# Kernel tuning notes

Measured on AMD Instinct MI355X. Metric: run time of the kernel, lower is better.

Reference implementation:

```python
import jax, jax.numpy as jnp
import numpy as np

R = 4  # num_relations


def rgcn_conv(x, src, dst, etype, W, root, bias):
    """PyG RGCNConv (aggr='mean', no self-loops):
    out_i = x_i @ root + bias + sum_r mean_{j in N_r(i)} (x_j @ W_r)
    x: [N,D], W: [R,D,H], root: [D,H], bias: [H]
    """
    N = x.shape[0]
    Rr, _, H = W.shape
    x_r = jnp.einsum('nd,rdh->rnh', x, W)          # [R,N,H] relation-transformed feats
    msg = x_r[etype, src]                          # [E,H] per-edge messages
    seg = etype * N + dst                          # combined (relation, dst) segment id
    sums = jax.ops.segment_sum(msg, seg, num_segments=Rr * N)            # [R*N,H]
    cnt = jax.ops.segment_sum(jnp.ones(msg.shape[0], msg.dtype), seg,
                              num_segments=Rr * N)                        # [R*N]
    mean = sums / jnp.maximum(cnt, 1.0)[:, None]
    agg = mean.reshape(Rr, N, H).sum(0)            # sum over relations
    return agg + x @ root + bias


def setup_inputs() -> dict:
    key = jax.random.key(0)
    ks = jax.random.split(key, 12)
    N, E, D, H, ED = 20000, 320000, 256, 256, 64
    s = lambda fan: 1.0 / np.sqrt(fan)
    return {
        'x': jax.random.normal(ks[0], (N, D), jnp.float32),
        'edge_index': jax.random.randint(ks[1], (2, E), 0, N),
        'edge_type': jax.random.randint(ks[2], (E,), 0, R),
        'edge_attr': jax.random.normal(ks[3], (E, ED), jnp.float32),
        'W0': jax.random.normal(ks[4], (R, D, H), jnp.float32) * s(D),
        'root0': jax.random.normal(ks[5], (D, H), jnp.float32) * s(D),
        'b0': jnp.zeros((H,), jnp.float32),
        'W1': jax.random.normal(ks[6], (R, H, H), jnp.float32) * s(H),
        'root1': jax.random.normal(ks[7], (H, H), jnp.float32) * s(H),
        'b1': jnp.zeros((H,), jnp.float32),
        'lin_w': jax.random.normal(ks[8], (H, 2), jnp.float32) * s(H),
        'lin_b': jnp.zeros((2,), jnp.float32),
    }


def reference(x, edge_index, edge_type, edge_attr, W0, root0, b0, W1, root1, b1, lin_w, lin_b):
    src, dst = edge_index[0], edge_index[1]
    h = jax.nn.relu(rgcn_conv(x, src, dst, edge_type, W0, root0, b0))
    h = rgcn_conv(h, src, dst, edge_type, W1, root1, b1)
    g = h.sum(axis=0, keepdims=True)   # global_add_pool, single graph -> [1,H]
    # dropout inactive in eval mode
    return g @ lin_w + lin_b           # [1,2]
```

## Files before the change

### kernel.cpp

```cpp
#include <hip/hip_runtime.h>
#include <hip/hip_bf16.h>

#define RREL 4
#define DIM 256
#define KDIM 1280
#define KMEAN 1024
#define BCAP 32

__device__ __forceinline__ float bf2f(unsigned short u) {
    union { unsigned int i; float f; } z; z.i = ((unsigned int)u) << 16; return z.f;
}
__device__ __forceinline__ unsigned short f2bf(float f) {
    __hip_bfloat16 h = __float2bfloat16(f);
    return *(unsigned short*)&h;
}

typedef __attribute__((ext_vector_type(8))) short bf16x8;
typedef __attribute__((ext_vector_type(8))) unsigned short u16x8;
typedef __attribute__((ext_vector_type(4))) float f32x4;
typedef __attribute__((ext_vector_type(4))) float fx4;


__global__ __launch_bounds__(256)
void prep(const int* __restrict__ etype, const int* __restrict__ src,
          const int* __restrict__ dst,
          int* __restrict__ counts, int* __restrict__ bucket, int N, int E,
          const float* __restrict__ x, __hip_bfloat16* __restrict__ xb, int n4,
          const float* __restrict__ W0, const float* __restrict__ root0,
          __hip_bfloat16* __restrict__ WT,
          int eb, int cb) {
    int b = blockIdx.x;
    if (b < eb) {
        int e = b * 256 + threadIdx.x;
        if (e < E) {
            int seg = etype[e] * N + dst[e];
            int p = atomicAdd(&counts[seg], 1);
            if (p < BCAP) bucket[(size_t)seg * BCAP + p] = src[e];
        }
    } else if (b < eb + cb) {
        int i = (b - eb) * 256 + threadIdx.x;
        if (i < n4) {
            fx4 v = *((const fx4*)x + i);
            ushort4 u = make_ushort4(f2bf(v.x), f2bf(v.y), f2bf(v.z), f2bf(v.w));
            ((ushort4*)xb)[i] = u;
        }
    } else {
        __shared__ float tile[32][33];
        int q = b - eb - cb;
        int nblk = q / 40;
        int kblk = q - nblk * 40;
        int k0 = kblk * 32, n0 = nblk * 32;
        int tx = threadIdx.x & 31, ty = threadIdx.x >> 5;
        const float* srcp;
        int kbase;
        if (k0 < RREL * DIM) { srcp = W0; kbase = k0; } else { srcp = root0; kbase = k0 - RREL * DIM; }
#pragma unroll
        for (int j = 0; j < 4; j++) {
            int k = kbase + ty + j * 8;
            tile[ty + j * 8][tx] = srcp[(size_t)k * DIM + n0 + tx];
        }
        __syncthreads();
#pragma unroll
        for (int j = 0; j < 4; j++) {
            int n = n0 + ty + j * 8;
            WT[(size_t)n * KDIM + k0 + tx] = __float2bfloat16(tile[tx][ty + j * 8]);
        }
    }
}


__global__ __launch_bounds__(256)
void aggregate(const __hip_bfloat16* __restrict__ feat, const int* __restrict__ counts,
               const int* __restrict__ bucket, __hip_bfloat16* __restrict__ Y, int N,
               const int* __restrict__ etype, const int* __restrict__ srcv,
               const int* __restrict__ dstv, float* __restrict__ wsr, int E, int ab) {
    if ((int)blockIdx.x >= ab) {
        int e = (blockIdx.x - ab) * 256 + threadIdx.x;
        if (e < E) {
            int r = etype[e];
            int seg = r * N + dstv[e];
            float sc = 1.f / (float)counts[seg];
            atomicAdd(&wsr[(size_t)srcv[e] * RREL + r], sc);
        }
        return;
    }
    int r = threadIdx.x >> 6, lane = threadIdx.x & 63;
    int h = lane >> 5, li = lane & 31;
    int i = blockIdx.x * 2 + h;
    if (i >= N) return;
    int seg = r * N + i;
    int cnt = min(counts[seg], BCAP);
    const unsigned short* fu = (const unsigned short*)feat;
    const int* bk = bucket + (size_t)seg * BCAP;
    float a[8] = {};
    for (int k = 0; k < cnt; k += 4) {
        int4 q = *(const int4*)(bk + k);
        float m1 = (k + 1 < cnt) ? 1.f : 0.f;
        float m2 = (k + 2 < cnt) ? 1.f : 0.f;
        float m3 = (k + 3 < cnt) ? 1.f : 0.f;
        int i0 = q.x;
        int i1 = m1 ? q.y : q.x;
        int i2 = m2 ? q.z : q.x;
        int i3 = m3 ? q.w : q.x;
        u16x8 v0 = *(const u16x8*)(fu + (size_t)i0 * DIM + li * 8);
        u16x8 v1 = *(const u16x8*)(fu + (size_t)i1 * DIM + li * 8);
        u16x8 v2 = *(const u16x8*)(fu + (size_t)i2 * DIM + li * 8);
        u16x8 v3 = *(const u16x8*)(fu + (size_t)i3 * DIM + li * 8);
#pragma unroll
        for (int j = 0; j < 8; j++)
            a[j] += bf2f(v0[j]) + m1 * bf2f(v1[j]) + m2 * bf2f(v2[j]) + m3 * bf2f(v3[j]);
    }
    float inv = (cnt > 0) ? 1.f / (float)cnt : 0.f;
    u16x8 u;
#pragma unroll
    for (int j = 0; j < 8; j++) u[j] = f2bf(a[j] * inv);
    __builtin_nontemporal_store(u,
        (u16x8*)((unsigned short*)Y + (size_t)i * KMEAN + r * DIM + li * 8));
}


#define BMg 64
#define BKg 32

__global__ __launch_bounds__(256)
void gemm_mfma(const __hip_bfloat16* __restrict__ A,
               const __hip_bfloat16* __restrict__ Aself,
               const __hip_bfloat16* __restrict__ Bt,
               const float* __restrict__ bias,
               const float* __restrict__ wsr,
               float* __restrict__ sv,
               int Nrows) {
    __shared__ short As[2][BMg * BKg];
    __shared__ short Bs[2][DIM * BKg];
    int t = threadIdx.x;
    int lane = t & 63;
    int w = t >> 6;
    size_t row0 = (size_t)blockIdx.x * BMg;

    const unsigned short* Ag = (const unsigned short*)A;
    const unsigned short* Sg = (const unsigned short*)Aself;
    const unsigned short* Bg = (const unsigned short*)Bt;

    float bb[4];
#pragma unroll
    for (int ni = 0; ni < 4; ni++) bb[ni] = bias[w * 64 + ni * 16 + (lane & 15)];

    f32x4 acc[4][4] = {};

    auto issue_tile = [&](int k0, short* as, short* bs) {
        const unsigned short* Abase;
        int kk, stride;
        if (k0 < KMEAN) { Abase = Ag; kk = k0; stride = KMEAN; }
        else            { Abase = Sg; kk = k0 - KMEAN; stride = DIM; }
        {
            int c = t;
            int r = c >> 2, pl = c & 3, pg = pl ^ (r & 3);
            const unsigned short* ga = Abase + (row0 + r) * stride + kk + pg * 8;
            __builtin_amdgcn_global_load_lds(
                (const __attribute__((address_space(1))) void*)ga,
                (__attribute__((address_space(3))) void*)((char*)as + c * 16),
                16, 0, 0);
        }
#pragma unroll
        for (int h = 0; h < 4; h++) {
            int c = t + h * 256;
            int r = c >> 2, pl = c & 3, pg = pl ^ (r & 3);
            const unsigned short* gb = Bg + (size_t)r * KDIM + k0 + pg * 8;
            __builtin_amdgcn_global_load_lds(
                (const __attribute__((address_space(1))) void*)gb,
                (__attribute__((address_space(3))) void*)((char*)bs + c * 16),
                16, 0, 0);
        }
    };

    issue_tile(0, As[0], Bs[0]);
    int cur = 0;
    for (int k0 = 0; k0 < KDIM; k0 += BKg) {
        if (k0 + BKg < KDIM) {
            issue_tile(k0 + BKg, As[cur ^ 1], Bs[cur ^ 1]);
            asm volatile("s_waitcnt vmcnt(5)" ::: "memory");
        } else {
            asm volatile("s_waitcnt vmcnt(0)" ::: "memory");
        }
        __builtin_amdgcn_s_barrier();
        __builtin_amdgcn_sched_barrier(0);
        const short* as = As[cur];
        const short* bs = Bs[cur];
        int p = lane >> 4;
        bf16x8 af[4], bfr[4];
#pragma unroll
        for (int mi = 0; mi < 4; mi++) {
            int m = mi * 16 + (lane & 15);
            af[mi] = *(const bf16x8*)&as[m * 32 + ((p ^ (m & 3)) * 8)];
        }
#pragma unroll
        for (int ni = 0; ni < 4; ni++) {
            int n = w * 64 + ni * 16 + (lane & 15);
            bfr[ni] = *(const bf16x8*)&bs[n * 32 + ((p ^ (n & 3)) * 8)];
        }
#pragma unroll
        for (int mi = 0; mi < 4; mi++)
#pragma unroll
            for (int ni = 0; ni < 4; ni++)
                acc[mi][ni] = __builtin_amdgcn_mfma_f32_16x16x32_bf16(af[mi], bfr[ni], acc[mi][ni], 0, 0, 0);
        __builtin_amdgcn_s_barrier();
        __builtin_amdgcn_sched_barrier(0);
        cur ^= 1;
    }

    float a[4][5];
#pragma unroll
    for (int ni = 0; ni < 4; ni++)
#pragma unroll
        for (int s = 0; s < 5; s++) a[ni][s] = 0.f;

#pragma unroll
    for (int mi = 0; mi < 4; mi++) {
#pragma unroll
        for (int j = 0; j < 4; j++) {
            size_t row = row0 + mi * 16 + (lane >> 4) * 4 + j;
            if (row < (size_t)Nrows) {
                fx4 wv = *(const fx4*)(wsr + row * RREL);
#pragma unroll
                for (int ni = 0; ni < 4; ni++) {
                    float v = fmaxf(acc[mi][ni][j] + bb[ni], 0.f);
                    a[ni][4] += v;
                    a[ni][0] += wv.x * v;
                    a[ni][1] += wv.y * v;
                    a[ni][2] += wv.z * v;
                    a[ni][3] += wv.w * v;
                }
            }
        }
    }
#pragma unroll
    for (int ni = 0; ni < 4; ni++) {
        int col = w * 64 + ni * 16 + (lane & 15);
#pragma unroll
        for (int s = 0; s < 5; s++) {
            float v = a[ni][s];
            v += __shfl_xor(v, 16, 64);
            v += __shfl_xor(v, 32, 64);
            if ((lane >> 4) == 0) atomicAdd(&sv[s * DIM + col], v);
        }
    }
}


__global__ __launch_bounds__(256)
void gemv_final(const float* __restrict__ sv, const float* __restrict__ W1,
                const float* __restrict__ root1, const float* __restrict__ b1,
                int N, float* __restrict__ g, int* __restrict__ done,
                const float* __restrict__ lw, const float* __restrict__ lb,
                float* __restrict__ out, int nblk) {
    int t = threadIdx.x;
    int kk0 = blockIdx.x * 8;
    float acc = 0.f;
#pragma unroll
    for (int u = 0; u < 8; u++) {
        int kk = kk0 + u;
        int r = kk >> 8;
        int k = kk & 255;
        const float* row = (r < RREL) ? (W1 + ((size_t)r * DIM + k) * DIM)
                                      : (root1 + (size_t)k * DIM);
        acc += sv[kk] * row[t];
    }
    if (blockIdx.x == 0) acc += (float)N * b1[t];
    atomicAdd(&g[t], acc);
    __threadfence();
    __shared__ int amLast;
    if (t == 0) amLast = (atomicAdd(done, 1) == nblk - 1);
    __syncthreads();
    if (!amLast) return;
    float gv = atomicAdd(&g[t], 0.f);
    __shared__ float s0[256], s1[256];
    s0[t] = gv * lw[t * 2 + 0];
    s1[t] = gv * lw[t * 2 + 1];
    __syncthreads();
    for (int off = 128; off > 0; off >>= 1) {
        if (t < off) { s0[t] += s0[t + off]; s1[t] += s1[t + off]; }
        __syncthreads();
    }
    if (t == 0) { out[0] = s0[0] + lb[0]; out[1] = s1[0] + lb[1]; }
}


static inline char* align_up(char* p, size_t a) {
    return (char*)(((uintptr_t)p + (a - 1)) & ~(uintptr_t)(a - 1));
}

extern "C" void kernel_launch(void* const* d_in, const int* in_sizes, int n_in,
                              void* d_out, int out_size, void* d_ws, size_t ws_size,
                              hipStream_t stream) {
    const float* x     = (const float*)d_in[0];
    const int*   eidx  = (const int*)d_in[1];
    const int*   etype = (const int*)d_in[2];
    const float* W0    = (const float*)d_in[4];
    const float* root0 = (const float*)d_in[5];
    const float* b0    = (const float*)d_in[6];
    const float* W1    = (const float*)d_in[7];
    const float* root1 = (const float*)d_in[8];
    const float* b1    = (const float*)d_in[9];
    const float* lin_w = (const float*)d_in[10];
    const float* lin_b = (const float*)d_in[11];
    float* out = (float*)d_out;

    const int N = in_sizes[0] / DIM;
    const int E = in_sizes[2];
    const int RN = RREL * N;
    const int* src = eidx;
    const int* dst = eidx + E;

    const int gx = (N + BMg - 1) / BMg;
    const int Mpad = gx * BMg;

    char* w = (char*)d_ws;
    int*   counts = (int*)w;   w += (size_t)RN * 4;
    float* wsr    = (float*)w; w += (size_t)N * RREL * 4;
    float* sv     = (float*)w; w += (size_t)5 * DIM * 4;
    float* g      = (float*)w; w += 256 * 4;
    int*   done   = (int*)w;   w += 256;
    size_t zero_bytes = (size_t)RN * 4 + (size_t)N * RREL * 4 + 5 * DIM * 4 + 256 * 4 + 256;
    int* bucket = (int*)w; w += (size_t)RN * BCAP * 4;
    w = align_up(w, 16);
    __hip_bfloat16* WT = (__hip_bfloat16*)w; w += (size_t)DIM * KDIM * 2;
    w = align_up(w, 16);
    __hip_bfloat16* Y  = (__hip_bfloat16*)w; w += (size_t)Mpad * KMEAN * 2;
    __hip_bfloat16* xb = (__hip_bfloat16*)w; w += (size_t)Mpad * DIM * 2;

    hipMemsetAsync(counts, 0, zero_bytes, stream);

    int eb = (E + 255) / 256;
    int n4 = N * DIM / 4;
    int cb = (n4 + 255) / 256;
    int wb = (KDIM / 32) * (DIM / 32);

    prep<<<eb + cb + wb, 256, 0, stream>>>(etype, src, dst, counts, bucket, N, E,
                                           x, xb, n4, W0, root0, WT, eb, cb);

    int ab = (N + 1) / 2;
    aggregate<<<ab + eb, 256, 0, stream>>>(xb, counts, bucket, Y, N,
                                           etype, src, dst, wsr, E, ab);
    gemm_mfma<<<gx, 256, 0, stream>>>(Y, xb, WT, b0, wsr, sv, N);
    int gvb = KDIM / 8;
    gemv_final<<<gvb, 256, 0, stream>>>(sv, W1, root1, b1, N, g, done,
                                        lin_w, lin_b, out, gvb);
}
```

Before: 255.5 us.

## Fuse neighbor-mean gather into MFMA GEMM prologue, drop intermediate Y buffer

Removes the separate aggregate kernel that wrote per-relation mean features to a large Y buffer. The GEMM now builds its A tiles itself by gathering neighbor rows from xb and averaging them in registers, then storing to LDS. The gather for the next K step overlaps with the MFMA work of the current one. The edge-weight atomics move to their own small kernel. This saves writing and re-reading Y, but puts irregular gather latency inside the GEMM loop, adds register pressure, and replaces async LDS loads for A with a full vmcnt(0) wait every step.

```diff
diff --git a/kernel.cpp b/kernel.cpp
--- a/kernel.cpp
+++ b/kernel.cpp
@@ -4,7 +4,6 @@
 #define RREL 4
 #define DIM 256
 #define KDIM 1280
-#define KMEAN 1024
 #define BCAP 32
 
 __device__ __forceinline__ float bf2f(unsigned short u) {
@@ -70,66 +69,32 @@
 
 
 __global__ __launch_bounds__(256)
-void aggregate(const __hip_bfloat16* __restrict__ feat, const int* __restrict__ counts,
-               const int* __restrict__ bucket, __hip_bfloat16* __restrict__ Y, int N,
-               const int* __restrict__ etype, const int* __restrict__ srcv,
-               const int* __restrict__ dstv, float* __restrict__ wsr, int E, int ab) {
-    if ((int)blockIdx.x >= ab) {
-        int e = (blockIdx.x - ab) * 256 + threadIdx.x;
-        if (e < E) {
-            int r = etype[e];
-            int seg = r * N + dstv[e];
-            float sc = 1.f / (float)counts[seg];
-            atomicAdd(&wsr[(size_t)srcv[e] * RREL + r], sc);
-        }
-        return;
-    }
-    int r = threadIdx.x >> 6, lane = threadIdx.x & 63;
-    int h = lane >> 5, li = lane & 31;
-    int i = blockIdx.x * 2 + h;
-    if (i >= N) return;
-    int seg = r * N + i;
-    int cnt = min(counts[seg], BCAP);
-    const unsigned short* fu = (const unsigned short*)feat;
-    const int* bk = bucket + (size_t)seg * BCAP;
-    float a[8] = {};
-    for (int k = 0; k < cnt; k += 4) {
-        int4 q = *(const int4*)(bk + k);
-        float m1 = (k + 1 < cnt) ? 1.f : 0.f;
-        float m2 = (k + 2 < cnt) ? 1.f : 0.f;
-        float m3 = (k + 3 < cnt) ? 1.f : 0.f;
-        int i0 = q.x;
-        int i1 = m1 ? q.y : q.x;
-        int i2 = m2 ? q.z : q.x;
-        int i3 = m3 ? q.w : q.x;
-        u16x8 v0 = *(const u16x8*)(fu + (size_t)i0 * DIM + li * 8);
-        u16x8 v1 = *(const u16x8*)(fu + (size_t)i1 * DIM + li * 8);
-        u16x8 v2 = *(const u16x8*)(fu + (size_t)i2 * DIM + li * 8);
-        u16x8 v3 = *(const u16x8*)(fu + (size_t)i3 * DIM + li * 8);
-#pragma unroll
-        for (int j = 0; j < 8; j++)
-            a[j] += bf2f(v0[j]) + m1 * bf2f(v1[j]) + m2 * bf2f(v2[j]) + m3 * bf2f(v3[j]);
-    }
-    float inv = (cnt > 0) ? 1.f / (float)cnt : 0.f;
-    u16x8 u;
-#pragma unroll
-    for (int j = 0; j < 8; j++) u[j] = f2bf(a[j] * inv);
-    __builtin_nontemporal_store(u,
-        (u16x8*)((unsigned short*)Y + (size_t)i * KMEAN + r * DIM + li * 8));
+void edgew(const int* __restrict__ etype, const int* __restrict__ srcv,
+           const int* __restrict__ dstv, const int* __restrict__ counts,
+           float* __restrict__ wsr, int N, int E) {
+    int e = blockIdx.x * 256 + threadIdx.x;
+    if (e < E) {
+        int r = etype[e];
+        int seg = r * N + dstv[e];
+        float sc = 1.f / (float)counts[seg];
+        atomicAdd(&wsr[(size_t)srcv[e] * RREL + r], sc);
+    }
 }
 
 
 #define BMg 64
 #define BKg 32
-
-__global__ __launch_bounds__(256)
-void gemm_mfma(const __hip_bfloat16* __restrict__ A,
-               const __hip_bfloat16* __restrict__ Aself,
-               const __hip_bfloat16* __restrict__ Bt,
-               const float* __restrict__ bias,
-               const float* __restrict__ wsr,
-               float* __restrict__ sv,
-               int Nrows) {
+#define NKS 40
+
+__global__ __launch_bounds__(256, 3)
+void gemm_fused(const __hip_bfloat16* __restrict__ xb,
+                const int* __restrict__ counts,
+                const int* __restrict__ bucket,
+                const __hip_bfloat16* __restrict__ Bt,
+                const float* __restrict__ bias,
+                const float* __restrict__ wsr,
+                float* __restrict__ sv,
+                int N) {
     __shared__ short As[2][BMg * BKg];
     __shared__ short Bs[2][DIM * BKg];
     int t = threadIdx.x;
@@ -137,30 +102,101 @@
     int w = t >> 6;
     size_t row0 = (size_t)blockIdx.x * BMg;
 
-    const unsigned short* Ag = (const unsigned short*)A;
-    const unsigned short* Sg = (const unsigned short*)Aself;
+    const unsigned short* fu = (const unsigned short*)xb;
     const unsigned short* Bg = (const unsigned short*)Bt;
 
+    int gi = t >> 2, td = t & 3;
+    size_t grow = row0 + gi;
+    int clampedrow = (grow < (size_t)N) ? (int)grow : (N - 1);
+
+    int cnt_r[5];
+    int4 q_r[5], q2_r[5];
+#pragma unroll
+    for (int r = 0; r < 4; r++) {
+        cnt_r[r] = 0;
+        if (grow < (size_t)N) cnt_r[r] = min(counts[r * N + (int)grow], BCAP);
+        const int* bk = bucket + ((size_t)r * N + clampedrow) * BCAP;
+        q_r[r]  = (cnt_r[r] > 0) ? *(const int4*)bk       : make_int4(0, 0, 0, 0);
+        q2_r[r] = (cnt_r[r] > 4) ? *(const int4*)(bk + 4) : make_int4(0, 0, 0, 0);
+    }
+    cnt_r[4] = 1;
+    q_r[4]  = make_int4((int)grow, 0, 0, 0);
+    q2_r[4] = make_int4(0, 0, 0, 0);
+
     float bb[4];
 #pragma unroll
     for (int ni = 0; ni < 4; ni++) bb[ni] = bias[w * 64 + ni * 16 + (lane & 15)];
 
     f32x4 acc[4][4] = {};
 
-    auto issue_tile = [&](int k0, short* as, short* bs) {
-        const unsigned short* Abase;
-        int kk, stride;
-        if (k0 < KMEAN) { Abase = Ag; kk = k0; stride = KMEAN; }
-        else            { Abase = Sg; kk = k0 - KMEAN; stride = DIM; }
-        {
-            int c = t;
-            int r = c >> 2, pl = c & 3, pg = pl ^ (r & 3);
-            const unsigned short* ga = Abase + (row0 + r) * stride + kk + pg * 8;
-            __builtin_amdgcn_global_load_lds(
-                (const __attribute__((address_space(1))) void*)ga,
-                (__attribute__((address_space(3))) void*)((char*)as + c * 16),
-                16, 0, 0);
-        }
+    struct G {
+        u16x8 v0, v1, v2, v3, v4, v5, v6, v7;
+        float m1, m2, m3, m4, m5, m6, m7;
+    };
+
+    auto g_issue = [&](int s, G& g) {
+        int r = s >> 3;
+        int d0 = (s & 7) * BKg;
+        int off = d0 + td * 8;
+        int c = cnt_r[r];
+        int4 q = q_r[r], q2 = q2_r[r];
+        g.m1 = (1 < c) ? 1.f : 0.f;  g.m2 = (2 < c) ? 1.f : 0.f;
+        g.m3 = (3 < c) ? 1.f : 0.f;  g.m4 = (4 < c) ? 1.f : 0.f;
+        g.m5 = (5 < c) ? 1.f : 0.f;  g.m6 = (6 < c) ? 1.f : 0.f;
+        g.m7 = (7 < c) ? 1.f : 0.f;
+        int i0 = q.x;
+        int i1 = g.m1 ? q.y  : i0;  int i2 = g.m2 ? q.z  : i0;
+        int i3 = g.m3 ? q.w  : i0;  int i4 = g.m4 ? q2.x : i0;
+        int i5 = g.m5 ? q2.y : i0;  int i6 = g.m6 ? q2.z : i0;
+        int i7 = g.m7 ? q2.w : i0;
+        g.v0 = *(const u16x8*)(fu + (size_t)i0 * DIM + off);
+        g.v1 = *(const u16x8*)(fu + (size_t)i1 * DIM + off);
+        g.v2 = *(const u16x8*)(fu + (size_t)i2 * DIM + off);
+        g.v3 = *(const u16x8*)(fu + (size_t)i3 * DIM + off);
+        g.v4 = *(const u16x8*)(fu + (size_t)i4 * DIM + off);
+        g.v5 = *(const u16x8*)(fu + (size_t)i5 * DIM + off);
+        g.v6 = *(const u16x8*)(fu + (size_t)i6 * DIM + off);
+        g.v7 = *(const u16x8*)(fu + (size_t)i7 * DIM + off);
+    };
+
+    auto g_finish = [&](int s, G& g, short* as) {
+        int r = s >> 3;
+        int d0 = (s & 7) * BKg;
+        int off = d0 + td * 8;
+        int c = cnt_r[r];
+        float a[8];
+#pragma unroll
+        for (int j = 0; j < 8; j++)
+            a[j] = bf2f(g.v0[j])
+                 + g.m1 * bf2f(g.v1[j]) + g.m2 * bf2f(g.v2[j]) + g.m3 * bf2f(g.v3[j])
+                 + g.m4 * bf2f(g.v4[j]) + g.m5 * bf2f(g.v5[j]) + g.m6 * bf2f(g.v6[j])
+                 + g.m7 * bf2f(g.v7[j]);
+        if (s < 32 && c > 8) {
+            const int* bk = bucket + ((size_t)(s >> 3) * N + clampedrow) * BCAP;
+            for (int kq = 8; kq < c; kq += 4) {
+                int4 q = *(const int4*)(bk + kq);
+                float n1 = (kq + 1 < c) ? 1.f : 0.f;
+                float n2 = (kq + 2 < c) ? 1.f : 0.f;
+                float n3 = (kq + 3 < c) ? 1.f : 0.f;
+                int i0 = q.x, i1 = n1 ? q.y : q.x, i2 = n2 ? q.z : q.x, i3 = n3 ? q.w : q.x;
+                u16x8 u0 = *(const u16x8*)(fu + (size_t)i0 * DIM + off);
+                u16x8 u1 = *(const u16x8*)(fu + (size_t)i1 * DIM + off);
+                u16x8 u2 = *(const u16x8*)(fu + (size_t)i2 * DIM + off);
+                u16x8 u3 = *(const u16x8*)(fu + (size_t)i3 * DIM + off);
+#pragma unroll
+                for (int j = 0; j < 8; j++)
+                    a[j] += bf2f(u0[j]) + n1 * bf2f(u1[j]) + n2 * bf2f(u2[j]) + n3 * bf2f(u3[j]);
+            }
+        }
+        float inv = (c > 0) ? 1.f / (float)c : 0.f;
+        u16x8 o;
+#pragma unroll
+        for (int j = 0; j < 8; j++) o[j] = f2bf(a[j] * inv);
+        *(u16x8*)&as[(td * 64 + gi) * 8] = o;
+    };
+
+    auto issue_B = [&](int s, short* bs) {
+        int k0 = s * BKg;
 #pragma unroll
         for (int h = 0; h < 4; h++) {
             int c = t + h * 256;
@@ -173,40 +209,48 @@
         }
     };
 
-    issue_tile(0, As[0], Bs[0]);
-    int cur = 0;
-    for (int k0 = 0; k0 < KDIM; k0 += BKg) {
-        if (k0 + BKg < KDIM) {
-            issue_tile(k0 + BKg, As[cur ^ 1], Bs[cur ^ 1]);
-            asm volatile("s_waitcnt vmcnt(5)" ::: "memory");
-        } else {
-            asm volatile("s_waitcnt vmcnt(0)" ::: "memory");
-        }
+    {
+        G g0;
+        g_issue(0, g0);
+        issue_B(0, Bs[0]);
+        g_finish(0, g0, As[0]);
+        asm volatile("s_waitcnt vmcnt(0) lgkmcnt(0)" ::: "memory");
         __builtin_amdgcn_s_barrier();
         __builtin_amdgcn_sched_barrier(0);
-        const short* as = As[cur];
-        const short* bs = Bs[cur];
+    }
+
+#pragma unroll
+    for (int s = 0; s < NKS; s++) {
+        const short* as_c = As[s & 1];
+        const short* bs_c = Bs[s & 1];
+        G g;
+        bool st = (s + 1 < NKS);
+        if (st) {
+            g_issue(s + 1, g);
+            issue_B(s + 1, (short*)Bs[(s + 1) & 1]);
+        }
         int p = lane >> 4;
         bf16x8 af[4], bfr[4];
 #pragma unroll
         for (int mi = 0; mi < 4; mi++) {
             int m = mi * 16 + (lane & 15);
-            af[mi] = *(const bf16x8*)&as[m * 32 + ((p ^ (m & 3)) * 8)];
+            af[mi] = *(const bf16x8*)&as_c[(p * 64 + m) * 8];
         }
 #pragma unroll
         for (int ni = 0; ni < 4; ni++) {
             int n = w * 64 + ni * 16 + (lane & 15);
-            bfr[ni] = *(const bf16x8*)&bs[n * 32 + ((p ^ (n & 3)) * 8)];
+            bfr[ni] = *(const bf16x8*)&bs_c[(n * 4 + (p ^ (n & 3))) * 8];
         }
 #pragma unroll
         for (int mi = 0; mi < 4; mi++)
 #pragma unroll
             for (int ni = 0; ni < 4; ni++)
                 acc[mi][ni] = __builtin_amdgcn_mfma_f32_16x16x32_bf16(af[mi], bfr[ni], acc[mi][ni], 0, 0, 0);
+        if (st) g_finish(s + 1, g, (short*)As[(s + 1) & 1]);
+        asm volatile("s_waitcnt vmcnt(0) lgkmcnt(0)" ::: "memory");
         __builtin_amdgcn_s_barrier();
         __builtin_amdgcn_sched_barrier(0);
-        cur ^= 1;
-    }
+        }
 
     float a[4][5];
 #pragma unroll
@@ -219,7 +263,7 @@
 #pragma unroll
         for (int j = 0; j < 4; j++) {
             size_t row = row0 + mi * 16 + (lane >> 4) * 4 + j;
-            if (row < (size_t)Nrows) {
+            if (row < (size_t)N) {
                 fx4 wv = *(const fx4*)(wsr + row * RREL);
 #pragma unroll
                 for (int ni = 0; ni < 4; ni++) {
@@ -325,7 +369,6 @@
     w = align_up(w, 16);
     __hip_bfloat16* WT = (__hip_bfloat16*)w; w += (size_t)DIM * KDIM * 2;
     w = align_up(w, 16);
-    __hip_bfloat16* Y  = (__hip_bfloat16*)w; w += (size_t)Mpad * KMEAN * 2;
     __hip_bfloat16* xb = (__hip_bfloat16*)w; w += (size_t)Mpad * DIM * 2;
 
     hipMemsetAsync(counts, 0, zero_bytes, stream);
@@ -338,10 +381,10 @@
     prep<<<eb + cb + wb, 256, 0, stream>>>(etype, src, dst, counts, bucket, N, E,
                                            x, xb, n4, W0, root0, WT, eb, cb);
 
-    int ab = (N + 1) / 2;
-    aggregate<<<ab + eb, 256, 0, stream>>>(xb, counts, bucket, Y, N,
-                                           etype, src, dst, wsr, E, ab);
-    gemm_mfma<<<gx, 256, 0, stream>>>(Y, xb, WT, b0, wsr, sv, N);
+    edgew<<<eb, 256, 0, stream>>>(etype, src, dst, counts, wsr, N, E);
+
+    gemm_fused<<<gx, 256, 0, stream>>>(xb, counts, bucket, WT, b0, wsr, sv, N);
+
     int gvb = KDIM / 8;
     gemv_final<<<gvb, 256, 0, stream>>>(sv, W1, root1, b1, N, g, done,
                                         lin_w, lin_b, out, gvb);
```

New measurement: 350.0 us. 37.0% more time.
